# Kernel optimization log

Hardware: AMD Instinct MI355X
Metric: run time of the kernel (lower is better)

Reference implementation:

```python
import jax, jax.numpy as jnp
import numpy as np

N_NODES = 100000   # number of graph nodes (users + items)
N_EDGES = 1600000  # nonzeros of the normalized adjacency (avg degree 16)
D_FEAT = 48        # node embedding dimension


def setup_inputs() -> dict:
    key = jax.random.key(0)
    k_t, k_x, k_r, k_c, k_v = jax.random.split(key, 5)
    t = jax.random.normal(k_t, (1,), dtype=jnp.float32)
    x = jax.random.normal(k_x, (N_NODES, D_FEAT), dtype=jnp.float32)
    # COO sparse adjacency: rows sorted (CSR-like ordering), random cols,
    # positive edge weights mimicking symmetric-normalized adjacency values.
    rows = jnp.sort(jax.random.randint(k_r, (N_EDGES,), 0, N_NODES, dtype=jnp.int32))
    cols = jax.random.randint(k_c, (N_EDGES,), 0, N_NODES, dtype=jnp.int32)
    vals = jax.random.uniform(k_v, (N_EDGES,), dtype=jnp.float32)
    return {"t": t, "x": x, "rows": rows, "cols": cols, "vals": vals}


def reference(t, x, rows, cols, vals):
    # torch.sparse.mm(graph, x): for each nonzero (r, c, v), out[r] += v * x[c].
    # t (ODE time) is unused by the module's forward.
    msgs = x[cols] * vals[:, None]                      # [E, D] gathered, scaled messages
    out = jax.ops.segment_sum(msgs, rows, num_segments=N_NODES)  # scatter-add to rows
    return out
```

## Files before the change

### kernel.cpp

```cpp
#include <hip/hip_runtime.h>
#include <hip/hip_bf16.h>
#include <hip/hip_fp16.h>


#define D_FEAT 48
#define TPR 12
#define RPB 16
#define BLOCK (TPR * RPB)

typedef float vfloat4 __attribute__((ext_vector_type(4)));

__global__ void build_row_ptr_scatter(const int* __restrict__ rows,
                                      int* __restrict__ row_ptr,
                                      int n_edges, int n_nodes) {
    int e = blockIdx.x * blockDim.x + threadIdx.x;
    if (e >= n_edges) return;
    const int r     = rows[e];
    const int rprev = (e == 0) ? -1 : rows[e - 1];
    for (int q = rprev + 1; q <= r; ++q) row_ptr[q] = e;
    if (e == n_edges - 1) {
        for (int q = r + 1; q <= n_nodes; ++q) row_ptr[q] = n_edges;
    }
}

__global__ void convert_x_f16(const float* __restrict__ x,
                              __half* __restrict__ xh, int n4) {
    int i = blockIdx.x * blockDim.x + threadIdx.x;
    if (i >= n4) return;
    const float4 f = reinterpret_cast<const float4*>(x)[i];
    union { ushort4 u; __half2 h2[2]; } pk;
    pk.h2[0] = __floats2half2_rn(f.x, f.y);
    pk.h2[1] = __floats2half2_rn(f.z, f.w);
    reinterpret_cast<ushort4*>(xh)[i] = pk.u;
}

__device__ __forceinline__ void fma4_h(vfloat4& acc, float v, const __half* p) {
    union { ushort4 u; __half2 h2[2]; } w;
    w.u = *reinterpret_cast<const ushort4*>(p);
    const float2 f0 = __half22float2(w.h2[0]);
    const float2 f1 = __half22float2(w.h2[1]);
    acc.x += v * f0.x;
    acc.y += v * f0.y;
    acc.z += v * f1.x;
    acc.w += v * f1.y;
}

__global__ __launch_bounds__(BLOCK) void spmm_rows_f16(
        const int* __restrict__ row_ptr,
        const int* __restrict__ cols,
        const float* __restrict__ vals,
        const __half* __restrict__ xh,
        float* __restrict__ out,
        int n_nodes) {
    const int tid = threadIdx.x;
    const int fg  = tid % TPR;
    const int rib = tid / TPR;
    const int r   = blockIdx.x * RPB + rib;
    if (r >= n_nodes) return;

    const int e0 = row_ptr[r];
    const int e1 = row_ptr[r + 1];

    vfloat4 acc = (vfloat4)(0.f);

    int e = e0;
    for (; e + 7 < e1; e += 8) {
        int   c[8];
        float v[8];
#pragma unroll
        for (int j = 0; j < 8; ++j) { c[j] = cols[e + j]; v[j] = vals[e + j]; }
#pragma unroll
        for (int j = 0; j < 8; ++j)
            fma4_h(acc, v[j], xh + (size_t)c[j] * D_FEAT + fg * 4);
    }
    for (; e + 3 < e1; e += 4) {
        int   c[4];
        float v[4];
#pragma unroll
        for (int j = 0; j < 4; ++j) { c[j] = cols[e + j]; v[j] = vals[e + j]; }
#pragma unroll
        for (int j = 0; j < 4; ++j)
            fma4_h(acc, v[j], xh + (size_t)c[j] * D_FEAT + fg * 4);
    }
    for (; e < e1; ++e) {
        fma4_h(acc, vals[e], xh + (size_t)cols[e] * D_FEAT + fg * 4);
    }

    __builtin_nontemporal_store(acc,
        reinterpret_cast<vfloat4*>(out + (size_t)r * D_FEAT + fg * 4));
}

__global__ __launch_bounds__(BLOCK) void spmm_rows_f32(
        const int* __restrict__ row_ptr,
        const int* __restrict__ cols,
        const float* __restrict__ vals,
        const float* __restrict__ x,
        float* __restrict__ out,
        int n_nodes) {
    const int tid = threadIdx.x;
    const int fg  = tid % TPR;
    const int rib = tid / TPR;
    const int r   = blockIdx.x * RPB + rib;
    if (r >= n_nodes) return;
    const int e0 = row_ptr[r];
    const int e1 = row_ptr[r + 1];
    float4 acc = make_float4(0.f, 0.f, 0.f, 0.f);
    for (int e = e0; e < e1; ++e) {
        const float v = vals[e];
        const float4 xa = *reinterpret_cast<const float4*>(
            x + (size_t)cols[e] * D_FEAT + fg * 4);
        acc.x += v * xa.x; acc.y += v * xa.y;
        acc.z += v * xa.z; acc.w += v * xa.w;
    }
    *reinterpret_cast<float4*>(out + (size_t)r * D_FEAT + fg * 4) = acc;
}

extern "C" void kernel_launch(void* const* d_in, const int* in_sizes, int n_in,
                              void* d_out, int out_size, void* d_ws, size_t ws_size,
                              hipStream_t stream) {
    const float* x    = (const float*)d_in[1];
    const int*   rows = (const int*)  d_in[2];
    const int*   cols = (const int*)  d_in[3];
    const float* vals = (const float*)d_in[4];
    float*       out  = (float*)d_out;

    const int n_edges = in_sizes[2];
    const int n_x     = in_sizes[1];
    const int n_nodes = out_size / D_FEAT;

    int* row_ptr = (int*)d_ws;
    const size_t rp_bytes  = (size_t)(n_nodes + 1) * sizeof(int);
    const size_t xh_off    = (rp_bytes + 255) & ~(size_t)255;
    const size_t need      = xh_off + (size_t)n_x * sizeof(__half);

    {
        const int threads = 256;
        const int grid = (n_edges + threads - 1) / threads;
        build_row_ptr_scatter<<<grid, threads, 0, stream>>>(rows, row_ptr, n_edges, n_nodes);
    }

    if (ws_size >= need) {
        __half* xh = (__half*)((char*)d_ws + xh_off);
        {
            const int n4 = n_x / 4;
            const int threads = 256;
            const int grid = (n4 + threads - 1) / threads;
            convert_x_f16<<<grid, threads, 0, stream>>>(x, xh, n4);
        }
        const int grid = (n_nodes + RPB - 1) / RPB;
        spmm_rows_f16<<<grid, BLOCK, 0, stream>>>(row_ptr, cols, vals, xh, out, n_nodes);
    } else {
        const int grid = (n_nodes + RPB - 1) / RPB;
        spmm_rows_f32<<<grid, BLOCK, 0, stream>>>(row_ptr, cols, vals, x, out, n_nodes);
    }
}
```

Baseline: 127.2 us.

## Split fp16 feature table into two column halves processed by separate blocks

The fp16 copy of x is stored as two separate 24-wide half-tables, and each SpMM block handles one half of the feature columns for 32 rows. Block indices are interleaved so that blocks for the same rows but different halves run close together in time. The aim is to shrink the working set each gather touches (48-byte rows instead of 96) so it fits L2/MALL better. In exchange, cols, vals and row_ptr are read twice, and each gather now fetches less than a full cache line.

```diff
diff --git a/kernel.cpp b/kernel.cpp
--- a/kernel.cpp
+++ b/kernel.cpp
@@ -4,9 +4,10 @@
 
 
 #define D_FEAT 48
-#define TPR 12
-#define RPB 16
-#define BLOCK (TPR * RPB)
+#define HALF_F 24
+#define TPR 6
+#define RPB 32
+#define BLOCK 192
 
 typedef float vfloat4 __attribute__((ext_vector_type(4)));
 
@@ -23,15 +24,21 @@
     }
 }
 
-__global__ void convert_x_f16(const float* __restrict__ x,
-                              __half* __restrict__ xh, int n4) {
+__global__ void convert_x_f16_split(const float* __restrict__ x,
+                                    __half* __restrict__ xh0,
+                                    __half* __restrict__ xh1, int n4) {
     int i = blockIdx.x * blockDim.x + threadIdx.x;
     if (i >= n4) return;
     const float4 f = reinterpret_cast<const float4*>(x)[i];
     union { ushort4 u; __half2 h2[2]; } pk;
     pk.h2[0] = __floats2half2_rn(f.x, f.y);
     pk.h2[1] = __floats2half2_rn(f.z, f.w);
-    reinterpret_cast<ushort4*>(xh)[i] = pk.u;
+    const int node = i / 12;
+    const int fg   = i % 12;
+    __half* dst = (fg < 6)
+        ? (xh0 + (size_t)node * HALF_F + fg * 4)
+        : (xh1 + (size_t)node * HALF_F + (fg - 6) * 4);
+    *reinterpret_cast<ushort4*>(dst) = pk.u;
 }
 
 __device__ __forceinline__ void fma4_h(vfloat4& acc, float v, const __half* p) {
@@ -45,18 +52,25 @@
     acc.w += v * f1.y;
 }
 
-__global__ __launch_bounds__(BLOCK) void spmm_rows_f16(
+__global__ __launch_bounds__(BLOCK) void spmm_half(
         const int* __restrict__ row_ptr,
         const int* __restrict__ cols,
         const float* __restrict__ vals,
-        const __half* __restrict__ xh,
+        const __half* __restrict__ xh0,
+        const __half* __restrict__ xh1,
         float* __restrict__ out,
         int n_nodes) {
+    const int g   = blockIdx.x;
+    const int oct = g & 7;
+    const int h   = oct >> 2;
+    const int rowblock = ((g >> 3) << 2) + (oct & 3);
     const int tid = threadIdx.x;
     const int fg  = tid % TPR;
     const int rib = tid / TPR;
-    const int r   = blockIdx.x * RPB + rib;
+    const int r   = rowblock * RPB + rib;
     if (r >= n_nodes) return;
+
+    const __half* __restrict__ xh = h ? xh1 : xh0;
 
     const int e0 = row_ptr[r];
     const int e1 = row_ptr[r + 1];
@@ -71,7 +85,7 @@
         for (int j = 0; j < 8; ++j) { c[j] = cols[e + j]; v[j] = vals[e + j]; }
 #pragma unroll
         for (int j = 0; j < 8; ++j)
-            fma4_h(acc, v[j], xh + (size_t)c[j] * D_FEAT + fg * 4);
+            fma4_h(acc, v[j], xh + (size_t)c[j] * HALF_F + fg * 4);
     }
     for (; e + 3 < e1; e += 4) {
         int   c[4];
@@ -80,14 +94,14 @@
         for (int j = 0; j < 4; ++j) { c[j] = cols[e + j]; v[j] = vals[e + j]; }
 #pragma unroll
         for (int j = 0; j < 4; ++j)
-            fma4_h(acc, v[j], xh + (size_t)c[j] * D_FEAT + fg * 4);
+            fma4_h(acc, v[j], xh + (size_t)c[j] * HALF_F + fg * 4);
     }
     for (; e < e1; ++e) {
-        fma4_h(acc, vals[e], xh + (size_t)cols[e] * D_FEAT + fg * 4);
+        fma4_h(acc, vals[e], xh + (size_t)cols[e] * HALF_F + fg * 4);
     }
 
     __builtin_nontemporal_store(acc,
-        reinterpret_cast<vfloat4*>(out + (size_t)r * D_FEAT + fg * 4));
+        reinterpret_cast<vfloat4*>(out + (size_t)r * D_FEAT + h * HALF_F + fg * 4));
 }
 
 __global__ __launch_bounds__(BLOCK) void spmm_rows_f32(
@@ -98,9 +112,9 @@
         float* __restrict__ out,
         int n_nodes) {
     const int tid = threadIdx.x;
-    const int fg  = tid % TPR;
-    const int rib = tid / TPR;
-    const int r   = blockIdx.x * RPB + rib;
+    const int fg  = tid % 12;
+    const int rib = tid / 12;
+    const int r   = blockIdx.x * 16 + rib;
     if (r >= n_nodes) return;
     const int e0 = row_ptr[r];
     const int e1 = row_ptr[r + 1];
@@ -129,9 +143,11 @@
     const int n_nodes = out_size / D_FEAT;
 
     int* row_ptr = (int*)d_ws;
-    const size_t rp_bytes  = (size_t)(n_nodes + 1) * sizeof(int);
-    const size_t xh_off    = (rp_bytes + 255) & ~(size_t)255;
-    const size_t need      = xh_off + (size_t)n_x * sizeof(__half);
+    const size_t rp_bytes   = (size_t)(n_nodes + 1) * sizeof(int);
+    const size_t xh0_off    = (rp_bytes + 255) & ~(size_t)255;
+    const size_t half_bytes = (size_t)n_nodes * HALF_F * sizeof(__half);
+    const size_t xh1_off    = (xh0_off + half_bytes + 255) & ~(size_t)255;
+    const size_t need       = xh1_off + half_bytes;
 
     {
         const int threads = 256;
@@ -140,17 +156,20 @@
     }
 
     if (ws_size >= need) {
-        __half* xh = (__half*)((char*)d_ws + xh_off);
+        __half* xh0 = (__half*)((char*)d_ws + xh0_off);
+        __half* xh1 = (__half*)((char*)d_ws + xh1_off);
         {
             const int n4 = n_x / 4;
             const int threads = 256;
             const int grid = (n4 + threads - 1) / threads;
-            convert_x_f16<<<grid, threads, 0, stream>>>(x, xh, n4);
+            convert_x_f16_split<<<grid, threads, 0, stream>>>(x, xh0, xh1, n4);
         }
-        const int grid = (n_nodes + RPB - 1) / RPB;
-        spmm_rows_f16<<<grid, BLOCK, 0, stream>>>(row_ptr, cols, vals, xh, out, n_nodes);
+        const int nrb  = (n_nodes + RPB - 1) / RPB;
+        const int nrb4 = (nrb + 3) & ~3;
+        const int grid = nrb4 * 2;
+        spmm_half<<<grid, BLOCK, 0, stream>>>(row_ptr, cols, vals, xh0, xh1, out, n_nodes);
     } else {
-        const int grid = (n_nodes + RPB - 1) / RPB;
+        const int grid = (n_nodes + 15) / 16;
         spmm_rows_f32<<<grid, BLOCK, 0, stream>>>(row_ptr, cols, vals, x, out, n_nodes);
     }
 }
```

After: 129.9 us. 1.02x slower.
